# Performance work log

Measured on AMD Instinct MI355X. Metric: run time of the kernel, lower is better.

## Reference

```python
import jax, jax.numpy as jnp
import numpy as np

HIDDEN_DIM = 256
ATTN_DIM = 256


def setup_inputs() -> dict:
    key = jax.random.key(0)
    k1, k2, k3, k4, k5, k6 = jax.random.split(key, 6)
    B, S, C, H, W = 16, 32, HIDDEN_DIM, 16, 16
    hidden_state = jax.random.normal(k1, (B, C, H, W), dtype=jnp.float32)
    encoder_outputs = jax.random.normal(k2, (B, S, C, H, W), dtype=jnp.float32)
    # 1x1 conv weights stored as [out_ch, in_ch] (kernel spatial dims are 1)
    W1 = jax.random.normal(k3, (ATTN_DIM, 2 * C), dtype=jnp.float32) * (1.0 / np.sqrt(2 * C))
    b1 = jax.random.normal(k4, (ATTN_DIM,), dtype=jnp.float32) * 0.01
    W2 = jax.random.normal(k5, (1, ATTN_DIM), dtype=jnp.float32) * (1.0 / np.sqrt(ATTN_DIM))
    b2 = jax.random.normal(k6, (1,), dtype=jnp.float32) * 0.01
    return {"hidden_state": hidden_state, "encoder_outputs": encoder_outputs,
            "W1": W1, "b1": b1, "W2": W2, "b2": b2}


def reference(hidden_state, encoder_outputs, W1, b1, W2, b2):
    # hidden_state: [B, C, H, W]; encoder_outputs: [B, S, C, H, W]
    C = hidden_state.shape[1]
    # conv1(cat(h_expanded, e)) decomposed: W1 = [W1h | W1e] over channel dim.
    W1h, W1e = W1[:, :C], W1[:, C:]
    # [B, A, H, W] broadcast over S + [B, S, A, H, W]
    eh = jnp.einsum('ac,bchw->bahw', W1h, hidden_state)
    ee = jnp.einsum('ac,bschw->bsahw', W1e, encoder_outputs)
    t = jnp.tanh(eh[:, None] + ee + b1[None, None, :, None, None])
    # conv2 -> [B, S, H, W], then spatial mean -> [B, S]
    energy = jnp.einsum('a,bsahw->bshw', W2[0], t) + b2[0]
    energy = energy.reshape(energy.shape[0], energy.shape[1], -1).mean(axis=2)
    attn_weights = jax.nn.softmax(energy, axis=1)  # [B, S]
    context = jnp.einsum('bs,bschw->bchw', attn_weights, encoder_outputs)
    return context
```

## Files before the change

### kernel.cpp

```cpp
#include <hip/hip_runtime.h>

#define P 256
#define CDIM 256
#define SDIM 32

typedef __attribute__((ext_vector_type(8))) short short8;
typedef __attribute__((ext_vector_type(4))) float f32x4;
typedef __attribute__((ext_vector_type(4))) unsigned int uint4v;

__device__ inline unsigned int pack2bf(float lo, float hi) {
    unsigned int ul = __builtin_bit_cast(unsigned int, lo);
    unsigned int uh = __builtin_bit_cast(unsigned int, hi);
    ul += 0x7fffu + ((ul >> 16) & 1u);
    uh += 0x7fffu + ((uh >> 16) & 1u);
    return (ul >> 16) | (uh & 0xffff0000u);
}

__global__ __launch_bounds__(256) void pack_w1e(const float* __restrict__ W1,
                                                uint4v* __restrict__ packA) {
    const int t  = blockIdx.x * 256 + threadIdx.x;
    const int a  = ((t >> 9) << 4) | (t & 15);
    const int kc = (t >> 4) & 31;
    const float* src = W1 + (size_t)a * 512 + 256 + kc * 8;
    const float4 f0 = *(const float4*)src;
    const float4 f1 = *(const float4*)(src + 4);
    uint4v u;
    u.x = pack2bf(f0.x, f0.y);
    u.y = pack2bf(f0.z, f0.w);
    u.z = pack2bf(f1.x, f1.y);
    u.w = pack2bf(f1.z, f1.w);
    packA[t] = u;
}

__global__ __launch_bounds__(256) void eh_kernel(const float* __restrict__ hid,
                                                 const float* __restrict__ W1,
                                                 const float* __restrict__ b1,
                                                 float* __restrict__ ehb1) {
    const int bi = blockIdx.x;
    const int b  = bi >> 5;
    const int a0 = (bi & 31) << 3;
    const int p  = threadIdx.x;
    float acc[8];
#pragma unroll
    for (int i = 0; i < 8; ++i) acc[i] = 0.f;
    const float* hb = hid + (size_t)b * CDIM * P;
    for (int c = 0; c < CDIM; c += 8) {
        float hv[8];
#pragma unroll
        for (int j = 0; j < 8; ++j) hv[j] = hb[(c + j) * P + p];
#pragma unroll
        for (int i = 0; i < 8; ++i) {
            const float* wr = W1 + (size_t)(a0 + i) * 512 + c;
#pragma unroll
            for (int j = 0; j < 8; ++j) acc[i] = fmaf(wr[j], hv[j], acc[i]);
        }
    }
#pragma unroll
    for (int i = 0; i < 8; ++i)
        ehb1[((size_t)b * CDIM + a0 + i) * P + p] = acc[i] + b1[a0 + i];
}

__global__ __launch_bounds__(256, 3) void energy_mfma(const float* __restrict__ enc,
                                                      const unsigned char* __restrict__ packA,
                                                      const float* __restrict__ W2,
                                                      const float* __restrict__ ehb1,
                                                      float* __restrict__ partial) {
    __shared__ __align__(16) unsigned char ldsB[2][64 * 128];
    __shared__ float red[4];
    const int bid = blockIdx.x;
    const int bs  = bid >> 2;
    const int pq  = bid & 3;
    const int b   = bs >> 5;
    const int tid = threadIdx.x;
    const int l   = tid & 63;
    const int w   = tid >> 6;
    const int g   = l >> 4;
    const int i16 = l & 15;
    const int a_base = w * 64;
    const int p_l = tid & 63;
    const int cq  = tid >> 6;
    const int swz = (p_l & 7) << 4;
    const float* eb = enc + (size_t)bs * (CDIM * P) + pq * 64;

    f32x4 acc[4][4];
#pragma unroll
    for (int m = 0; m < 4; ++m)
#pragma unroll
        for (int n = 0; n < 4; ++n) acc[m][n] = (f32x4){0.f, 0.f, 0.f, 0.f};

    {
        const float* src = eb + (size_t)(cq * 16) * P + p_l;
        float v[16];
#pragma unroll
        for (int j = 0; j < 16; ++j) v[j] = src[(size_t)j * P];
        unsigned char* dst = ldsB[0] + p_l * 128;
#pragma unroll
        for (int h = 0; h < 2; ++h) {
            uint4v u;
            u.x = pack2bf(v[h*8+0], v[h*8+1]);
            u.y = pack2bf(v[h*8+2], v[h*8+3]);
            u.z = pack2bf(v[h*8+4], v[h*8+5]);
            u.w = pack2bf(v[h*8+6], v[h*8+7]);
            *(uint4v*)(dst + ((cq * 32 + h * 16) ^ swz)) = u;
        }
    }
    __syncthreads();

#pragma unroll
    for (int kt = 0; kt < 4; ++kt) {
        short8 af[2][4];
#pragma unroll
        for (int kh = 0; kh < 2; ++kh)
#pragma unroll
            for (int m = 0; m < 4; ++m) {
                const int chunk = ((a_base >> 4) + m) * 32 + kt * 8 + kh * 4;
                af[kh][m] = __builtin_bit_cast(short8,
                    *(const uint4v*)(packA + (size_t)chunk * 256 + l * 16));
            }
        float v[16];
        if (kt < 3) {
            const float* src = eb + (size_t)((kt + 1) * 64 + cq * 16) * P + p_l;
#pragma unroll
            for (int j = 0; j < 16; ++j) v[j] = src[(size_t)j * P];
        }
#pragma unroll
        for (int kh = 0; kh < 2; ++kh) {
            short8 bf[4];
#pragma unroll
            for (int n = 0; n < 4; ++n) {
                const int row = n * 16 + i16;
                bf[n] = __builtin_bit_cast(short8,
                    *(const uint4v*)(ldsB[kt & 1] + row * 128 +
                                     (((kh * 4 + g) * 16) ^ ((row & 7) << 4))));
            }
#pragma unroll
            for (int m = 0; m < 4; ++m)
#pragma unroll
                for (int n = 0; n < 4; ++n)
                    acc[m][n] = __builtin_amdgcn_mfma_f32_16x16x32_bf16(af[kh][m], bf[n], acc[m][n], 0, 0, 0);
        }
        if (kt < 3) {
            unsigned char* dst = ldsB[(kt + 1) & 1] + p_l * 128;
#pragma unroll
            for (int h = 0; h < 2; ++h) {
                uint4v u;
                u.x = pack2bf(v[h*8+0], v[h*8+1]);
                u.y = pack2bf(v[h*8+2], v[h*8+3]);
                u.z = pack2bf(v[h*8+4], v[h*8+5]);
                u.w = pack2bf(v[h*8+6], v[h*8+7]);
                *(uint4v*)(dst + ((cq * 32 + h * 16) ^ swz)) = u;
            }
            __syncthreads();
        }
    }

    float ep = 0.f;
    const float* ehbB = ehb1 + (size_t)b * (CDIM * P);
#pragma unroll
    for (int m = 0; m < 4; ++m) {
#pragma unroll
        for (int r = 0; r < 4; ++r) {
            const int a = a_base + m * 16 + g * 4 + r;
            const float w2v = W2[a];
            const float* ehr = ehbB + (size_t)a * P + pq * 64 + i16;
#pragma unroll
            for (int n = 0; n < 4; ++n) {
                const float x  = acc[m][n][r] + ehr[n * 16];
                const float ex = __expf(2.f * x);
                const float t  = 1.f - 2.f / (ex + 1.f);
                ep = fmaf(w2v, t, ep);
            }
        }
    }
#pragma unroll
    for (int off = 32; off > 0; off >>= 1) ep += __shfl_down(ep, off, 64);
    if (l == 0) red[w] = ep;
    __syncthreads();
    if (tid == 0)
        partial[(size_t)bs * 4 + pq] = red[0] + red[1] + red[2] + red[3];
}

__global__ __launch_bounds__(256) void context_kernel(const float4* __restrict__ enc4,
                                                      const float* __restrict__ partial,
                                                      const float* __restrict__ b2,
                                                      float4* __restrict__ out4) {
    const int bi = blockIdx.x;
    const int b  = bi >> 6;
    const int i4 = ((bi & 63) << 8) + threadIdx.x;

    float e[SDIM];
    const float* pb = partial + (size_t)b * SDIM * 4;
    const float bias = b2[0];
#pragma unroll
    for (int s = 0; s < SDIM; ++s)
        e[s] = (pb[s*4] + pb[s*4+1] + pb[s*4+2] + pb[s*4+3]) * (1.f / 256.f) + bias;
    float m = e[0];
#pragma unroll
    for (int s = 1; s < SDIM; ++s) m = fmaxf(m, e[s]);
    float sum = 0.f;
#pragma unroll
    for (int s = 0; s < SDIM; ++s) { e[s] = __expf(e[s] - m); sum += e[s]; }
    const float inv = 1.f / sum;

    float4 acc = {0.f, 0.f, 0.f, 0.f};
    const float4* eb = enc4 + (size_t)b * SDIM * 16384 + i4;
#pragma unroll 4
    for (int s = 0; s < SDIM; ++s) {
        const float wv = e[s] * inv;
        const float4 v = eb[(size_t)s * 16384];
        acc.x = fmaf(wv, v.x, acc.x);
        acc.y = fmaf(wv, v.y, acc.y);
        acc.z = fmaf(wv, v.z, acc.z);
        acc.w = fmaf(wv, v.w, acc.w);
    }
    out4[(size_t)b * 16384 + i4] = acc;
}

extern "C" void kernel_launch(void* const* d_in, const int* in_sizes, int n_in,
                              void* d_out, int out_size, void* d_ws, size_t ws_size,
                              hipStream_t stream) {
    const float* hid = (const float*)d_in[0];
    const float* enc = (const float*)d_in[1];
    const float* W1  = (const float*)d_in[2];
    const float* b1  = (const float*)d_in[3];
    const float* W2  = (const float*)d_in[4];
    const float* b2  = (const float*)d_in[5];
    float* out = (float*)d_out;

    float* ehb1    = out;
    float* partial = (float*)d_ws;
    unsigned char* packA = (unsigned char*)(partial + 2048);

    pack_w1e<<<32, 256, 0, stream>>>(W1, (uint4v*)packA);
    eh_kernel<<<512, 256, 0, stream>>>(hid, W1, b1, ehb1);
    energy_mfma<<<2048, 256, 0, stream>>>(enc, packA, W2, ehb1, partial);
    context_kernel<<<1024, 256, 0, stream>>>((const float4*)enc, partial, b2, (float4*)out);
}
```

Measured before the change: 99.99 us.

## Stage encoder tiles via float4 loads and fp32 LDS transpose; merge prep kernels

The energy kernel now loads encoder tiles with 16-byte float4 global reads into a swizzled fp32 LDS buffer. It then transposes them through LDS before packing to bf16, replacing the previous per-thread scalar strided loads. The two setup kernels (W1e packing and eh computation) are merged into one launch to cut a kernel launch. The cost is an extra 16KB of LDS per block, which may reduce occupancy, plus an additional barrier per k-tile.

```diff
diff --git a/kernel.cpp b/kernel.cpp
--- a/kernel.cpp
+++ b/kernel.cpp
@@ -16,30 +16,31 @@
     return (ul >> 16) | (uh & 0xffff0000u);
 }
 
-__global__ __launch_bounds__(256) void pack_w1e(const float* __restrict__ W1,
-                                                uint4v* __restrict__ packA) {
-    const int t  = blockIdx.x * 256 + threadIdx.x;
-    const int a  = ((t >> 9) << 4) | (t & 15);
-    const int kc = (t >> 4) & 31;
-    const float* src = W1 + (size_t)a * 512 + 256 + kc * 8;
-    const float4 f0 = *(const float4*)src;
-    const float4 f1 = *(const float4*)(src + 4);
-    uint4v u;
-    u.x = pack2bf(f0.x, f0.y);
-    u.y = pack2bf(f0.z, f0.w);
-    u.z = pack2bf(f1.x, f1.y);
-    u.w = pack2bf(f1.z, f1.w);
-    packA[t] = u;
-}
-
-__global__ __launch_bounds__(256) void eh_kernel(const float* __restrict__ hid,
-                                                 const float* __restrict__ W1,
-                                                 const float* __restrict__ b1,
-                                                 float* __restrict__ ehb1) {
-    const int bi = blockIdx.x;
-    const int b  = bi >> 5;
-    const int a0 = (bi & 31) << 3;
-    const int p  = threadIdx.x;
+__global__ __launch_bounds__(256) void prep_kernel(const float* __restrict__ hid,
+                                                   const float* __restrict__ W1,
+                                                   const float* __restrict__ b1,
+                                                   float* __restrict__ ehb1,
+                                                   uint4v* __restrict__ packA) {
+    const int blk = blockIdx.x;
+    const int tid = threadIdx.x;
+    if (blk >= 512) {
+        const int t  = (blk - 512) * 256 + tid;
+        const int a  = ((t >> 9) << 4) | (t & 15);
+        const int kc = (t >> 4) & 31;
+        const float* src = W1 + (size_t)a * 512 + 256 + kc * 8;
+        const float4 f0 = *(const float4*)src;
+        const float4 f1 = *(const float4*)(src + 4);
+        uint4v u;
+        u.x = pack2bf(f0.x, f0.y);
+        u.y = pack2bf(f0.z, f0.w);
+        u.z = pack2bf(f1.x, f1.y);
+        u.w = pack2bf(f1.z, f1.w);
+        packA[t] = u;
+        return;
+    }
+    const int b  = blk >> 5;
+    const int a0 = (blk & 31) << 3;
+    const int p  = tid;
     float acc[8];
 #pragma unroll
     for (int i = 0; i < 8; ++i) acc[i] = 0.f;
@@ -65,6 +66,7 @@
                                                       const float* __restrict__ W2,
                                                       const float* __restrict__ ehb1,
                                                       float* __restrict__ partial) {
+    __shared__ __align__(16) unsigned char ldsF[64 * 256];
     __shared__ __align__(16) unsigned char ldsB[2][64 * 128];
     __shared__ float red[4];
     const int bid = blockIdx.x;
@@ -77,9 +79,10 @@
     const int g   = l >> 4;
     const int i16 = l & 15;
     const int a_base = w * 64;
-    const int p_l = tid & 63;
-    const int cq  = tid >> 6;
-    const int swz = (p_l & 7) << 4;
+    const int cg4 = tid >> 4;
+    const int p4  = tid & 15;
+    const int p_r = tid & 63;
+    const int ch  = tid >> 6;
     const float* eb = enc + (size_t)bs * (CDIM * P) + pq * 64;
 
     f32x4 acc[4][4];
@@ -89,25 +92,46 @@
         for (int n = 0; n < 4; ++n) acc[m][n] = (f32x4){0.f, 0.f, 0.f, 0.f};
 
     {
-        const float* src = eb + (size_t)(cq * 16) * P + p_l;
-        float v[16];
-#pragma unroll
-        for (int j = 0; j < 16; ++j) v[j] = src[(size_t)j * P];
-        unsigned char* dst = ldsB[0] + p_l * 128;
+        float4 gv[4];
+#pragma unroll
+        for (int r = 0; r < 4; ++r)
+            gv[r] = *(const float4*)(eb + (size_t)(r * 16 + cg4) * P + p4 * 4);
+#pragma unroll
+        for (int r = 0; r < 4; ++r) {
+            const int c = r * 16 + cg4;
+            *(float4*)(ldsF + c * 256 + ((p4 * 16) ^ ((c & 7) << 4))) = gv[r];
+        }
+    }
+    __syncthreads();
+    {
+        float cv[16];
+#pragma unroll
+        for (int j = 0; j < 16; ++j) {
+            const int c = ch * 16 + j;
+            cv[j] = *(const float*)(ldsF + c * 256 +
+                     ((((p_r >> 2) * 16) ^ ((c & 7) << 4)) | ((p_r & 3) * 4)));
+        }
+        unsigned char* dst = ldsB[0] + p_r * 128;
 #pragma unroll
         for (int h = 0; h < 2; ++h) {
             uint4v u;
-            u.x = pack2bf(v[h*8+0], v[h*8+1]);
-            u.y = pack2bf(v[h*8+2], v[h*8+3]);
-            u.z = pack2bf(v[h*8+4], v[h*8+5]);
-            u.w = pack2bf(v[h*8+6], v[h*8+7]);
-            *(uint4v*)(dst + ((cq * 32 + h * 16) ^ swz)) = u;
+            u.x = pack2bf(cv[h*8+0], cv[h*8+1]);
+            u.y = pack2bf(cv[h*8+2], cv[h*8+3]);
+            u.z = pack2bf(cv[h*8+4], cv[h*8+5]);
+            u.w = pack2bf(cv[h*8+6], cv[h*8+7]);
+            *(uint4v*)(dst + ((ch * 32 + h * 16) ^ ((p_r & 7) << 4))) = u;
         }
     }
     __syncthreads();
 
 #pragma unroll
     for (int kt = 0; kt < 4; ++kt) {
+        float4 gv[4];
+        if (kt < 3) {
+#pragma unroll
+            for (int r = 0; r < 4; ++r)
+                gv[r] = *(const float4*)(eb + (size_t)((kt + 1) * 64 + r * 16 + cg4) * P + p4 * 4);
+        }
         short8 af[2][4];
 #pragma unroll
         for (int kh = 0; kh < 2; ++kh)
@@ -117,12 +141,6 @@
                 af[kh][m] = __builtin_bit_cast(short8,
                     *(const uint4v*)(packA + (size_t)chunk * 256 + l * 16));
             }
-        float v[16];
-        if (kt < 3) {
-            const float* src = eb + (size_t)((kt + 1) * 64 + cq * 16) * P + p_l;
-#pragma unroll
-            for (int j = 0; j < 16; ++j) v[j] = src[(size_t)j * P];
-        }
 #pragma unroll
         for (int kh = 0; kh < 2; ++kh) {
             short8 bf[4];
@@ -140,15 +158,28 @@
                     acc[m][n] = __builtin_amdgcn_mfma_f32_16x16x32_bf16(af[kh][m], bf[n], acc[m][n], 0, 0, 0);
         }
         if (kt < 3) {
-            unsigned char* dst = ldsB[(kt + 1) & 1] + p_l * 128;
+#pragma unroll
+            for (int r = 0; r < 4; ++r) {
+                const int c = r * 16 + cg4;
+                *(float4*)(ldsF + c * 256 + ((p4 * 16) ^ ((c & 7) << 4))) = gv[r];
+            }
+            __syncthreads();
+            float cv[16];
+#pragma unroll
+            for (int j = 0; j < 16; ++j) {
+                const int c = ch * 16 + j;
+                cv[j] = *(const float*)(ldsF + c * 256 +
+                         ((((p_r >> 2) * 16) ^ ((c & 7) << 4)) | ((p_r & 3) * 4)));
+            }
+            unsigned char* dst = ldsB[(kt + 1) & 1] + p_r * 128;
 #pragma unroll
             for (int h = 0; h < 2; ++h) {
                 uint4v u;
-                u.x = pack2bf(v[h*8+0], v[h*8+1]);
-                u.y = pack2bf(v[h*8+2], v[h*8+3]);
-                u.z = pack2bf(v[h*8+4], v[h*8+5]);
-                u.w = pack2bf(v[h*8+6], v[h*8+7]);
-                *(uint4v*)(dst + ((cq * 32 + h * 16) ^ swz)) = u;
+                u.x = pack2bf(cv[h*8+0], cv[h*8+1]);
+                u.y = pack2bf(cv[h*8+2], cv[h*8+3]);
+                u.z = pack2bf(cv[h*8+4], cv[h*8+5]);
+                u.w = pack2bf(cv[h*8+6], cv[h*8+7]);
+                *(uint4v*)(dst + ((ch * 32 + h * 16) ^ ((p_r & 7) << 4))) = u;
             }
             __syncthreads();
         }
@@ -231,8 +262,7 @@
     float* partial = (float*)d_ws;
     unsigned char* packA = (unsigned char*)(partial + 2048);
 
-    pack_w1e<<<32, 256, 0, stream>>>(W1, (uint4v*)packA);
-    eh_kernel<<<512, 256, 0, stream>>>(hid, W1, b1, ehb1);
+    prep_kernel<<<544, 256, 0, stream>>>(hid, W1, b1, ehb1, (uint4v*)packA);
     energy_mfma<<<2048, 256, 0, stream>>>(enc, packA, W2, ehb1, partial);
     context_kernel<<<1024, 256, 0, stream>>>((const float4*)enc, partial, b2, (float4*)out);
 }
```

Measured after the change: 104.0 us. 1.04x slower.
